# Kernel optimization log

Hardware: AMD Instinct MI355X
Metric: run time of the kernel (lower is better)

## Reference

```python
import jax, jax.numpy as jnp
import numpy as np
from jax import lax

TAU = 2.0
V_TH = 1.0
ALPHA = 4.0   # spikingjelly surrogate.Sigmoid default
BN_EPS = 1e-5
HEADS = 8


def lif(x):
    """Multi-step LIF neuron (tau=2, v_reset=0, hard reset, detach_reset).
    x: [T, ...] -> spikes [T, ...]. Forward is Heaviside; sigmoid surrogate
    is wired in via straight-through for the bwd variant."""
    def step(v, xt):
        v = v + (xt - v) / TAU                      # charge
        sg = jax.nn.sigmoid(ALPHA * (v - V_TH))     # surrogate
        hard = (v >= V_TH).astype(x.dtype)
        spike = sg + lax.stop_gradient(hard - sg)   # fwd: hard, bwd: sigmoid'
        v = v * (1.0 - lax.stop_gradient(spike))    # detached hard reset to 0
        return v, spike
    _, s = lax.scan(step, jnp.zeros_like(x[0]), x)
    return s


def conv1x1_bn(x, w, g, b, m, var, bias=None):
    # x: [N, C, H, W]; 1x1 conv == channel matmul, then eval-mode BN
    y = jnp.einsum('nchw,dc->ndhw', x, w)
    if bias is not None:
        y = y + bias[None, :, None, None]
    scale = g / jnp.sqrt(var + BN_EPS)
    shift = b - m * scale
    return y * scale[None, :, None, None] + shift[None, :, None, None]


def to_heads(x, T, B, C, H, W):
    # [T,B,C,H,W] -> [T,B,heads,N,hd]
    N = H * W
    hd = C // HEADS
    x = x.reshape(T, B, C, N).transpose(0, 1, 3, 2)          # [T,B,N,C]
    return x.reshape(T, B, N, HEADS, hd).transpose(0, 1, 3, 2, 4)


def _forward(x, q_w, q_bn_g, q_bn_b, q_bn_m, q_bn_v,
             k_w, k_bn_g, k_bn_b, k_bn_m, k_bn_v,
             v_w, v_bn_g, v_bn_b, v_bn_m, v_bn_v,
             out_w, out_b, out_bn_g, out_bn_b, out_bn_m, out_bn_v):
    T, B, C, H, W = x.shape
    N = H * W
    identity = x

    xs = lif(x)                                  # shortcut_lif
    x_qkv = xs.reshape(T * B, C, H, W)

    q = lif(conv1x1_bn(x_qkv, q_w, q_bn_g, q_bn_b, q_bn_m, q_bn_v).reshape(T, B, C, H, W))
    k = lif(conv1x1_bn(x_qkv, k_w, k_bn_g, k_bn_b, k_bn_m, k_bn_v).reshape(T, B, C, H, W))
    v = lif(conv1x1_bn(x_qkv, v_w, v_bn_g, v_bn_b, v_bn_m, v_bn_v).reshape(T, B, C, H, W))

    qh = to_heads(q, T, B, C, H, W)              # [T,B,h,N,hd]
    kh = to_heads(k, T, B, C, H, W)
    vh = to_heads(v, T, B, C, H, W)

    kv = jnp.sum(kh * vh, axis=-2, keepdims=True)   # [T,B,h,1,hd]
    kv = lif(kv)                                    # talking_heads_proj_lif
    y = qh * kv                                     # [T,B,h,N,hd]

    # [T,B,h,N,hd] -> transpose(3,4) -> [T,B,h,hd,N] -> [T,B,C,H,W]
    y = y.transpose(0, 1, 2, 4, 3).reshape(T, B, C, H, W)
    y = conv1x1_bn(y.reshape(T * B, C, H, W), out_w, out_bn_g, out_bn_b,
                   out_bn_m, out_bn_v, bias=out_b).reshape(T, B, C, H, W)
    return y + identity, vh


def setup_inputs() -> dict:
    key = jax.random.key(0)
    ks = jax.random.split(key, 6)
    T, B, C, H, W = 4, 32, 512, 14, 14
    inp = {
        'x': jax.random.normal(ks[0], (T, B, C, H, W), dtype=jnp.float32),
        'q_w': jax.random.normal(ks[1], (C, C), dtype=jnp.float32) * 0.05,
        'k_w': jax.random.normal(ks[2], (C, C), dtype=jnp.float32) * 0.05,
        'v_w': jax.random.normal(ks[3], (C, C), dtype=jnp.float32) * 0.05,
        'out_w': jax.random.normal(ks[4], (C, C), dtype=jnp.float32) * 0.05,
        'out_b': jnp.zeros((C,), dtype=jnp.float32),
    }
    for p in ('q', 'k', 'v', 'out'):
        inp[f'{p}_bn_g'] = jnp.ones((C,), dtype=jnp.float32)
        inp[f'{p}_bn_b'] = jnp.zeros((C,), dtype=jnp.float32)
        inp[f'{p}_bn_m'] = jnp.zeros((C,), dtype=jnp.float32)
        inp[f'{p}_bn_v'] = jnp.ones((C,), dtype=jnp.float32)
    return inp


def reference(x, q_w, q_bn_g, q_bn_b, q_bn_m, q_bn_v,
              k_w, k_bn_g, k_bn_b, k_bn_m, k_bn_v,
              v_w, v_bn_g, v_bn_b, v_bn_m, v_bn_v,
              out_w, out_b, out_bn_g, out_bn_b, out_bn_m, out_bn_v):
    return _forward(x, q_w, q_bn_g, q_bn_b, q_bn_m, q_bn_v,
                    k_w, k_bn_g, k_bn_b, k_bn_m, k_bn_v,
                    v_w, v_bn_g, v_bn_b, v_bn_m, v_bn_v,
                    out_w, out_b, out_bn_g, out_bn_b, out_bn_m, out_bn_v)
```

## Files before the change

### kernel.cpp

```cpp
#include <hip/hip_runtime.h>
#include <math.h>

#define T_   4
#define B_   32
#define C_   512
#define N_   196
#define TB_  128
#define M_   25088
#define BNP_ 6272
#define OUT1_ 12845056

typedef unsigned short ushort_t;
typedef __attribute__((ext_vector_type(8)))  __bf16 bf16x8;
typedef __attribute__((ext_vector_type(16))) float  f32x16;

__device__ __forceinline__ ushort_t f2bf(float f) {
    unsigned int u = __float_as_uint(f);
    u = u + 0x7FFFu + ((u >> 16) & 1u);
    return (ushort_t)(u >> 16);
}
__device__ __forceinline__ float bf2f(ushort_t h) {
    return __uint_as_float(((unsigned int)h) << 16);
}

#define GL2LDS(gp, lp) \
    __builtin_amdgcn_global_load_lds((const __attribute__((address_space(1))) void*)(gp), \
                                     (__attribute__((address_space(3))) void*)(lp), 16, 0, 0)

__global__ void prep_kernel(
    const float* __restrict__ qw, const float* __restrict__ kw,
    const float* __restrict__ vw, const float* __restrict__ ow,
    const float* __restrict__ qg, const float* __restrict__ qb, const float* __restrict__ qm, const float* __restrict__ qv,
    const float* __restrict__ kg, const float* __restrict__ kb, const float* __restrict__ km, const float* __restrict__ kvr,
    const float* __restrict__ vg, const float* __restrict__ vb, const float* __restrict__ vm, const float* __restrict__ vv,
    const float* __restrict__ og, const float* __restrict__ ob, const float* __restrict__ om, const float* __restrict__ ov,
    const float* __restrict__ obias,
    ushort_t* __restrict__ wsplit, ushort_t* __restrict__ osplit,
    float* __restrict__ scale_qkv, float* __restrict__ shift_qkv,
    float* __restrict__ scale_o,   float* __restrict__ shift_o,
    float* __restrict__ kvpart)
{
    int i = blockIdx.x * 256 + threadIdx.x;
    int d = i >> 9, c = i & 511;
    const float* src = (d < 512) ? qw : (d < 1024) ? kw : vw;
    float wv = src[(d & 511) * 512 + c];
    ushort_t h = f2bf(wv);
    float r1 = wv - bf2f(h);
    ushort_t mm = f2bf(r1);
    wsplit[((size_t)d * 2 + 0) * 512 + c] = h;
    wsplit[((size_t)d * 2 + 1) * 512 + c] = mm;
    if (d < 512)
        osplit[(size_t)d * 512 + c] = f2bf(ow[d * 512 + c]);

    if (i < 3 * C_) {
        int p = i >> 9, dl = i & 511;
        const float* g = (p == 0) ? qg : (p == 1) ? kg : vg;
        const float* b = (p == 0) ? qb : (p == 1) ? kb : vb;
        const float* m = (p == 0) ? qm : (p == 1) ? km : vm;
        const float* r = (p == 0) ? qv : (p == 1) ? kvr : vv;
        float sc = g[dl] / sqrtf(r[dl] + 1e-5f);
        scale_qkv[i] = sc;
        shift_qkv[i] = b[dl] - m[dl] * sc;
    }
    if (i < C_) {
        float sc = og[i] / sqrtf(ov[i] + 1e-5f);
        scale_o[i] = sc;
        shift_o[i] = ob[i] - om[i] * sc + obias[i] * sc;
    }
    if (i < TB_ * C_) kvpart[i] = 0.f;
}

__global__ __launch_bounds__(256)
void lifx_kernel(const float* __restrict__ x, ushort_t* __restrict__ xs)
{
    __shared__ ushort_t tile[64 * 66];
    const int tid = threadIdx.x;
    const int b = blockIdx.z, c0 = blockIdx.y * 64, n0 = blockIdx.x * 64;
    const int j = tid & 63, w = tid >> 6;
    const bool nok = (n0 + j) < N_;
    float v[16];
#pragma unroll
    for (int r = 0; r < 16; ++r) v[r] = 0.f;
    for (int t = 0; t < T_; ++t) {
        const float* xb = x + ((size_t)((t * B_ + b) * C_ + c0)) * N_ + n0 + j;
#pragma unroll
        for (int r = 0; r < 16; ++r) {
            int i = w * 16 + r;
            float xv = nok ? xb[(size_t)i * N_] : 0.f;
            v[r] = v[r] + (xv - v[r]) * 0.5f;
            bool s = (v[r] >= 1.0f);
            tile[j * 66 + i] = s ? 0x3F80 : 0;
            if (s) v[r] = 0.f;
        }
        __syncthreads();
#pragma unroll
        for (int p = 0; p < 2; ++p) {
            int w2 = tid + p * 256;
            int jj = w2 >> 3, ck = w2 & 7;
            if (n0 + jj < N_) {
                const unsigned int* src = reinterpret_cast<const unsigned int*>(&tile[jj * 66 + ck * 8]);
                uint4 dv; dv.x = src[0]; dv.y = src[1]; dv.z = src[2]; dv.w = src[3];
                size_t mp = (size_t)(b * N_ + n0 + jj) * 4 + t;
                *reinterpret_cast<uint4*>(&xs[mp * 512 + c0 + ck * 8]) = dv;
            }
        }
        __syncthreads();
    }
}

__global__ __launch_bounds__(512, 4)
void qkv_gemm_lif(const ushort_t* __restrict__ W, const ushort_t* __restrict__ X,
                  const float* __restrict__ scale, const float* __restrict__ shift,
                  ushort_t* __restrict__ spk, float* __restrict__ out2)
{
    const int id = blockIdx.x;
    const int xw = id & 7, local = id >> 3;
    const int ml = local / 12, d_t = local - ml * 12;
    const int m_t = ml * 8 + xw;
    if (m_t >= 98) return;
    const int m0 = m_t * 256;
    const int d0 = d_t * 128;

    __shared__ ushort_t Xs[2][16 * 512];
    __shared__ ushort_t Ws[2][16 * 512];
    const int tid = threadIdx.x, wid = tid >> 6, lane = tid & 63;
    const int mw = (wid & 3) * 64, dw = (wid >> 2) * 64;
    const int row32 = lane & 31, khalf = lane >> 5;

    f32x16 acc[2][2] = {};

    auto STAGE = [&](int buf, int k0) {
        {
            int q = wid, mb = q >> 1, ks = q & 1;
            const ushort_t* g = X + (size_t)(m0 + mb * 32 + row32) * 512 + k0 + ks * 16 + khalf * 8;
            GL2LDS(g, &Xs[buf][q * 512]);
        }
        {
            int q = wid + 8, mb = q >> 1, ks = q & 1;
            const ushort_t* g = X + (size_t)(m0 + mb * 32 + row32) * 512 + k0 + ks * 16 + khalf * 8;
            GL2LDS(g, &Xs[buf][q * 512]);
        }
        {
            int q = wid, s = q >> 3, rem = q & 7, db = rem >> 1, ks = rem & 1;
            const ushort_t* g = W + ((size_t)(d0 + db * 32 + row32) * 2 + s) * 512 + k0 + ks * 16 + khalf * 8;
            GL2LDS(g, &Ws[buf][q * 512]);
        }
        {
            int q = wid + 8, s = q >> 3, rem = q & 7, db = rem >> 1, ks = rem & 1;
            const ushort_t* g = W + ((size_t)(d0 + db * 32 + row32) * 2 + s) * 512 + k0 + ks * 16 + khalf * 8;
            GL2LDS(g, &Ws[buf][q * 512]);
        }
    };

    STAGE(0, 0);
    __syncthreads();
    int cur = 0;

    for (int it = 0; it < 16; ++it) {
        if (it < 15) STAGE(cur ^ 1, (it + 1) * 32);

        __builtin_amdgcn_s_setprio(1);
#pragma unroll
        for (int ks = 0; ks < 2; ++ks) {
            bf16x8 xfr[2];
#pragma unroll
            for (int i = 0; i < 2; ++i)
                xfr[i] = *reinterpret_cast<const bf16x8*>(
                    &Xs[cur][(((mw >> 5) + i) * 2 + ks) * 512 + lane * 8]);
#pragma unroll
            for (int s = 0; s < 2; ++s)
#pragma unroll
                for (int j = 0; j < 2; ++j) {
                    bf16x8 wfr = *reinterpret_cast<const bf16x8*>(
                        &Ws[cur][(s * 8 + ((dw >> 5) + j) * 2 + ks) * 512 + lane * 8]);
#pragma unroll
                    for (int i = 0; i < 2; ++i)
                        acc[i][j] = __builtin_amdgcn_mfma_f32_32x32x16_bf16(xfr[i], wfr, acc[i][j], 0, 0, 0);
                }
        }
        __builtin_amdgcn_s_setprio(0);

        __syncthreads();
        cur ^= 1;
    }

    const int p = d0 >> 9;
    const bool isV = (p == 2);
    ushort_t* plane = spk + (size_t)p * ((size_t)M_ * 512);
#pragma unroll
    for (int j = 0; j < 2; ++j) {
        int d = d0 + dw + j * 32 + row32;
        float sc = scale[d], sh = shift[d];
        int dl = d & 511;
        int h = dl >> 6, hd = dl & 63;
#pragma unroll
        for (int i = 0; i < 2; ++i) {
            int bnb = (m0 + mw + i * 32) >> 2;
            f32x16 a = acc[i][j];
#pragma unroll
            for (int g = 0; g < 4; ++g) {
                int bn = bnb + 2 * g + khalf;
                float p0 = fmaf(a[4 * g + 0], sc, sh);
                float p1 = fmaf(a[4 * g + 1], sc, sh);
                float p2 = fmaf(a[4 * g + 2], sc, sh);
                float p3 = fmaf(a[4 * g + 3], sc, sh);
                float v = p0 * 0.5f;
                bool s0 = (v >= 1.f); if (s0) v = 0.f;
                v = v + (p1 - v) * 0.5f;
                bool s1 = (v >= 1.f); if (s1) v = 0.f;
                v = v + (p2 - v) * 0.5f;
                bool s2 = (v >= 1.f); if (s2) v = 0.f;
                v = v + (p3 - v) * 0.5f;
                bool s3 = (v >= 1.f);
                ushort_t* b0 = plane + (size_t)bn * 512 + dl;
                b0[0]                      = s0 ? 0x3F80 : 0;
                b0[(size_t)BNP_ * 512]     = s1 ? 0x3F80 : 0;
                b0[(size_t)2 * BNP_ * 512] = s2 ? 0x3F80 : 0;
                b0[(size_t)3 * BNP_ * 512] = s3 ? 0x3F80 : 0;
                if (isV) {
                    int b = bn / N_, n = bn - b * N_;
                    float* o = out2 + (((size_t)b * 8 + h) * N_ + n) * 64 + hd;
                    o[0]                       = s0 ? 1.f : 0.f;
                    o[(size_t)1 * (OUT1_ / 4)] = s1 ? 1.f : 0.f;
                    o[(size_t)2 * (OUT1_ / 4)] = s2 ? 1.f : 0.f;
                    o[(size_t)3 * (OUT1_ / 4)] = s3 ? 1.f : 0.f;
                }
            }
        }
    }
}

__global__ void kv_part_kernel(const ushort_t* __restrict__ ks, const ushort_t* __restrict__ vs,
                               float* __restrict__ kvpart)
{
    int id = blockIdx.x;
    int tb = id >> 3, r = id & 7;
    int c  = (r & 1) * 256 + threadIdx.x;
    int n0 = (r >> 1) * 49;
    const ushort_t* kb = ks + (size_t)tb * N_ * 512 + c;
    const ushort_t* vb = vs + (size_t)tb * N_ * 512 + c;
    int cnt = 0;
    for (int n = n0; n < n0 + 49; ++n)
        cnt += (kb[(size_t)n * 512] & vb[(size_t)n * 512]) ? 1 : 0;
    atomicAdd(&kvpart[tb * 512 + c], (float)cnt);
}

__global__ void kv_lif_kernel(const float* __restrict__ kvpart, ushort_t* __restrict__ kvs)
{
    int i = blockIdx.x * 256 + threadIdx.x;
    if (i >= B_ * C_) return;
    int b = i >> 9, c = i & 511;
    float v = 0.f;
#pragma unroll
    for (int t = 0; t < T_; ++t) {
        float y = kvpart[((t * B_ + b) << 9) + c];
        v = v + (y - v) * 0.5f;
        bool s = (v >= 1.f);
        kvs[((t * B_ + b) << 9) + c] = s ? 0x3F80 : 0;
        if (s) v = 0.f;
    }
}

__global__ __launch_bounds__(256)
void out_gemm(const ushort_t* __restrict__ A, const ushort_t* __restrict__ qs,
              const ushort_t* __restrict__ kvs,
              const float* __restrict__ scale, const float* __restrict__ shift,
              const float* __restrict__ xid, float* __restrict__ out)
{
    const int id = blockIdx.x;
    const int xw = id & 7, local = id >> 3;
    const int m_t = (local >> 2) * 8 + xw, d_t = local & 3;
    if (m_t >= 196) return;
    const int m0 = m_t * 128, d0 = d_t * 128;

    __shared__ ushort_t As[8 * 512];
    __shared__ ushort_t Bs[8 * 512];
    const int tid = threadIdx.x, wid = tid >> 6, lane = tid & 63;
    const int dw = (wid >> 1) * 64, mw = (wid & 1) * 64;
    const int row32 = lane & 31, khalf = lane >> 5;

    int sm[2], stb[2], sq[2], sL[2];
#pragma unroll
    for (int u = 0; u < 2; ++u) {
        int s = tid + u * 256;
        sq[u] = s >> 6; sL[u] = s & 63;
        sm[u] = m0 + (sq[u] >> 1) * 32 + (sL[u] & 31);
        stb[u] = sm[u] / N_;
    }

    f32x16 acc[2][2] = {};

    for (int k0 = 0; k0 < 512; k0 += 32) {
        __syncthreads();
        for (int q = wid; q < 8; q += 4) {
            int db = q >> 1, ks = q & 1;
            const ushort_t* g = A + (size_t)(d0 + db * 32 + row32) * 512 + k0 + ks * 16 + khalf * 8;
            GL2LDS(g, &As[q * 512]);
        }
#pragma unroll
        for (int u = 0; u < 2; ++u) {
            int kk = k0 + (sq[u] & 1) * 16 + (sL[u] >> 5) * 8;
            uint4 qv = *reinterpret_cast<const uint4*>(&qs[(size_t)sm[u] * 512 + kk]);
            uint4 kv = *reinterpret_cast<const uint4*>(&kvs[(size_t)stb[u] * 512 + kk]);
            uint4 o; o.x = qv.x & kv.x; o.y = qv.y & kv.y; o.z = qv.z & kv.z; o.w = qv.w & kv.w;
            *reinterpret_cast<uint4*>(&Bs[sq[u] * 512 + sL[u] * 8]) = o;
        }
        __syncthreads();

#pragma unroll
        for (int ks = 0; ks < 2; ++ks) {
            bf16x8 afr[2];
#pragma unroll
            for (int i = 0; i < 2; ++i)
                afr[i] = *reinterpret_cast<const bf16x8*>(&As[(((dw >> 5) + i) * 2 + ks) * 512 + lane * 8]);
#pragma unroll
            for (int j = 0; j < 2; ++j) {
                bf16x8 bfr = *reinterpret_cast<const bf16x8*>(&Bs[(((mw >> 5) + j) * 2 + ks) * 512 + lane * 8]);
#pragma unroll
                for (int i = 0; i < 2; ++i)
                    acc[i][j] = __builtin_amdgcn_mfma_f32_32x32x16_bf16(afr[i], bfr, acc[i][j], 0, 0, 0);
            }
        }
    }

#pragma unroll
    for (int j = 0; j < 2; ++j) {
        int m = m0 + mw + j * 32 + row32;
        int tb = m / N_;
        int n  = m - tb * N_;
        size_t mbase = (size_t)tb * (C_ * N_) + n;
#pragma unroll
        for (int i = 0; i < 2; ++i) {
            int dbase = d0 + dw + i * 32 + 4 * khalf;
            f32x16 a = acc[i][j];
#pragma unroll
            for (int g = 0; g < 4; ++g) {
#pragma unroll
                for (int t = 0; t < 4; ++t) {
                    int d = dbase + t + 8 * g;
                    float val = fmaf(a[4 * g + t], scale[d], shift[d]);
                    size_t ad = mbase + (size_t)d * N_;
                    out[ad] = val + xid[ad];
                }
            }
        }
    }
}

extern "C" void kernel_launch(void* const* d_in, const int* in_sizes, int n_in,
                              void* d_out, int out_size, void* d_ws, size_t ws_size,
                              hipStream_t stream)
{
    const float* x    = (const float*)d_in[0];
    const float* q_w  = (const float*)d_in[1];
    const float* k_w  = (const float*)d_in[2];
    const float* v_w  = (const float*)d_in[3];
    const float* o_w  = (const float*)d_in[4];
    const float* o_b  = (const float*)d_in[5];
    const float* qg = (const float*)d_in[6],  *qb = (const float*)d_in[7],
               *qm = (const float*)d_in[8],  *qv = (const float*)d_in[9];
    const float* kg = (const float*)d_in[10], *kb = (const float*)d_in[11],
               *km = (const float*)d_in[12], *kv = (const float*)d_in[13];
    const float* vg = (const float*)d_in[14], *vb = (const float*)d_in[15],
               *vm = (const float*)d_in[16], *vv = (const float*)d_in[17];
    const float* og = (const float*)d_in[18], *ob = (const float*)d_in[19],
               *om = (const float*)d_in[20], *ov = (const float*)d_in[21];

    float* out1  = (float*)d_out;
    float* out2f = out1 + OUT1_;

    ushort_t* spk    = (ushort_t*)d_ws;
    ushort_t* xs     = spk + (size_t)3 * M_ * 512;
    ushort_t* wsplit = xs + (size_t)M_ * 512;
    ushort_t* osplit = wsplit + (size_t)1536 * 2 * 512;
    float*    kvpart = (float*)(osplit + (size_t)512 * 512);
    ushort_t* kvs    = (ushort_t*)(kvpart + TB_ * C_);
    float*    scq    = (float*)(kvs + TB_ * C_);
    float*    shq    = scq + 3 * C_;
    float*    sco    = shq + 3 * C_;
    float*    sho    = sco + C_;

    ushort_t* qsp = spk;
    ushort_t* ksp = spk + (size_t)M_ * 512;
    ushort_t* vsp = spk + (size_t)2 * M_ * 512;

    prep_kernel<<<(1536 * 512) / 256, 256, 0, stream>>>(
        q_w, k_w, v_w, o_w,
        qg, qb, qm, qv, kg, kb, km, kv, vg, vb, vm, vv, og, ob, om, ov, o_b,
        wsplit, osplit, scq, shq, sco, sho, kvpart);

    lifx_kernel<<<dim3(4, 8, 32), 256, 0, stream>>>(x, xs);

    qkv_gemm_lif<<<1200, 512, 0, stream>>>(wsplit, xs, scq, shq, spk, out2f);

    kv_part_kernel<<<1024, 256, 0, stream>>>(ksp, vsp, kvpart);

    kv_lif_kernel<<<64, 256, 0, stream>>>(kvpart, kvs);

    out_gemm<<<800, 256, 0, stream>>>(osplit, qsp, kvs, sco, sho, x, out1);
}
```

Before: 412.0 us.

## Double-buffer out_gemm, relax qkv_gemm barriers, vectorize kv reduction

The out_gemm kernel now double-buffers its A and B tiles in LDS, prefetching the next K slice from global memory while MFMAs run on the current one. qkv_gemm replaces full __syncthreads with explicit vmcnt/lgkmcnt waits and raw barriers, so the prefetch for the next stage can stay in flight. kv_part_kernel is rewritten to read 8 channels per thread with uint4 loads and reduce through LDS atomics, dropping the global float atomics and using fewer blocks. Doubling out_gemm's LDS may lower occupancy, and the hand-written waitcnt values must match the number of outstanding loads for results to stay correct.

```diff
diff --git a/kernel.cpp b/kernel.cpp
--- a/kernel.cpp
+++ b/kernel.cpp
@@ -130,34 +130,36 @@
     f32x16 acc[2][2] = {};
 
     auto STAGE = [&](int buf, int k0) {
-        {
-            int q = wid, mb = q >> 1, ks = q & 1;
+        {   int q = wid, mb = q >> 1, ks = q & 1;
             const ushort_t* g = X + (size_t)(m0 + mb * 32 + row32) * 512 + k0 + ks * 16 + khalf * 8;
             GL2LDS(g, &Xs[buf][q * 512]);
         }
-        {
-            int q = wid + 8, mb = q >> 1, ks = q & 1;
+        {   int q = wid + 8, mb = q >> 1, ks = q & 1;
             const ushort_t* g = X + (size_t)(m0 + mb * 32 + row32) * 512 + k0 + ks * 16 + khalf * 8;
             GL2LDS(g, &Xs[buf][q * 512]);
         }
-        {
-            int q = wid, s = q >> 3, rem = q & 7, db = rem >> 1, ks = rem & 1;
+        {   int q = wid, s = q >> 3, rem = q & 7, db = rem >> 1, ks = rem & 1;
             const ushort_t* g = W + ((size_t)(d0 + db * 32 + row32) * 2 + s) * 512 + k0 + ks * 16 + khalf * 8;
             GL2LDS(g, &Ws[buf][q * 512]);
         }
-        {
-            int q = wid + 8, s = q >> 3, rem = q & 7, db = rem >> 1, ks = rem & 1;
+        {   int q = wid + 8, s = q >> 3, rem = q & 7, db = rem >> 1, ks = rem & 1;
             const ushort_t* g = W + ((size_t)(d0 + db * 32 + row32) * 2 + s) * 512 + k0 + ks * 16 + khalf * 8;
             GL2LDS(g, &Ws[buf][q * 512]);
         }
     };
 
     STAGE(0, 0);
-    __syncthreads();
     int cur = 0;
 
     for (int it = 0; it < 16; ++it) {
-        if (it < 15) STAGE(cur ^ 1, (it + 1) * 32);
+        if (it < 15) {
+            STAGE(cur ^ 1, (it + 1) * 32);
+            asm volatile("s_waitcnt vmcnt(4)" ::: "memory");
+        } else {
+            asm volatile("s_waitcnt vmcnt(0)" ::: "memory");
+        }
+        __builtin_amdgcn_s_barrier();
+        __builtin_amdgcn_sched_barrier(0);
 
         __builtin_amdgcn_s_setprio(1);
 #pragma unroll
@@ -180,7 +182,8 @@
         }
         __builtin_amdgcn_s_setprio(0);
 
-        __syncthreads();
+        asm volatile("s_waitcnt lgkmcnt(0)" ::: "memory");
+        __builtin_amdgcn_s_barrier();
         cur ^= 1;
     }
 
@@ -230,19 +233,34 @@
     }
 }
 
-__global__ void kv_part_kernel(const ushort_t* __restrict__ ks, const ushort_t* __restrict__ vs,
-                               float* __restrict__ kvpart)
-{
-    int id = blockIdx.x;
-    int tb = id >> 3, r = id & 7;
-    int c  = (r & 1) * 256 + threadIdx.x;
-    int n0 = (r >> 1) * 49;
+__global__ __launch_bounds__(256)
+void kv_part_kernel(const ushort_t* __restrict__ ks, const ushort_t* __restrict__ vs,
+                    float* __restrict__ kvpart)
+{
+    __shared__ int cnt[256];
+    const int tid = threadIdx.x;
+    cnt[tid] = 0;
+    __syncthreads();
+    const int tb = blockIdx.x >> 1, ch = blockIdx.x & 1;
+    const int cg = tid & 31, ns = tid >> 5;
+    const int c = ch * 256 + cg * 8;
     const ushort_t* kb = ks + (size_t)tb * N_ * 512 + c;
     const ushort_t* vb = vs + (size_t)tb * N_ * 512 + c;
-    int cnt = 0;
-    for (int n = n0; n < n0 + 49; ++n)
-        cnt += (kb[(size_t)n * 512] & vb[(size_t)n * 512]) ? 1 : 0;
-    atomicAdd(&kvpart[tb * 512 + c], (float)cnt);
+    int loc[8] = {0, 0, 0, 0, 0, 0, 0, 0};
+    int n1 = ns * 25 + 25; if (n1 > N_) n1 = N_;
+    for (int n = ns * 25; n < n1; ++n) {
+        uint4 kq = *reinterpret_cast<const uint4*>(&kb[(size_t)n * 512]);
+        uint4 vq = *reinterpret_cast<const uint4*>(&vb[(size_t)n * 512]);
+        unsigned m;
+        m = kq.x & vq.x; loc[0] += (m & 0xFFFFu) ? 1 : 0; loc[1] += (m >> 16) ? 1 : 0;
+        m = kq.y & vq.y; loc[2] += (m & 0xFFFFu) ? 1 : 0; loc[3] += (m >> 16) ? 1 : 0;
+        m = kq.z & vq.z; loc[4] += (m & 0xFFFFu) ? 1 : 0; loc[5] += (m >> 16) ? 1 : 0;
+        m = kq.w & vq.w; loc[6] += (m & 0xFFFFu) ? 1 : 0; loc[7] += (m >> 16) ? 1 : 0;
+    }
+#pragma unroll
+    for (int e = 0; e < 8; ++e) atomicAdd(&cnt[cg * 8 + e], loc[e]);
+    __syncthreads();
+    kvpart[tb * 512 + ch * 256 + tid] = (float)cnt[tid];
 }
 
 __global__ void kv_lif_kernel(const float* __restrict__ kvpart, ushort_t* __restrict__ kvs)
@@ -273,8 +291,8 @@
     if (m_t >= 196) return;
     const int m0 = m_t * 128, d0 = d_t * 128;
 
-    __shared__ ushort_t As[8 * 512];
-    __shared__ ushort_t Bs[8 * 512];
+    __shared__ ushort_t As[2][8 * 512];
+    __shared__ ushort_t Bs[2][8 * 512];
     const int tid = threadIdx.x, wid = tid >> 6, lane = tid & 63;
     const int dw = (wid >> 1) * 64, mw = (wid & 1) * 64;
     const int row32 = lane & 31, khalf = lane >> 5;
@@ -290,37 +308,75 @@
 
     f32x16 acc[2][2] = {};
 
-    for (int k0 = 0; k0 < 512; k0 += 32) {
-        __syncthreads();
-        for (int q = wid; q < 8; q += 4) {
-            int db = q >> 1, ks = q & 1;
-            const ushort_t* g = A + (size_t)(d0 + db * 32 + row32) * 512 + k0 + ks * 16 + khalf * 8;
-            GL2LDS(g, &As[q * 512]);
-        }
+    {
+        uint4 o[2];
 #pragma unroll
         for (int u = 0; u < 2; ++u) {
-            int kk = k0 + (sq[u] & 1) * 16 + (sL[u] >> 5) * 8;
+            int kk = (sq[u] & 1) * 16 + (sL[u] >> 5) * 8;
             uint4 qv = *reinterpret_cast<const uint4*>(&qs[(size_t)sm[u] * 512 + kk]);
             uint4 kv = *reinterpret_cast<const uint4*>(&kvs[(size_t)stb[u] * 512 + kk]);
-            uint4 o; o.x = qv.x & kv.x; o.y = qv.y & kv.y; o.z = qv.z & kv.z; o.w = qv.w & kv.w;
-            *reinterpret_cast<uint4*>(&Bs[sq[u] * 512 + sL[u] * 8]) = o;
-        }
-        __syncthreads();
-
+            o[u].x = qv.x & kv.x; o[u].y = qv.y & kv.y;
+            o[u].z = qv.z & kv.z; o[u].w = qv.w & kv.w;
+        }
+        for (int q = wid; q < 8; q += 4) {
+            int db = q >> 1, ks2 = q & 1;
+            const ushort_t* g = A + (size_t)(d0 + db * 32 + row32) * 512 + ks2 * 16 + khalf * 8;
+            GL2LDS(g, &As[0][q * 512]);
+        }
+#pragma unroll
+        for (int u = 0; u < 2; ++u)
+            *reinterpret_cast<uint4*>(&Bs[0][sq[u] * 512 + sL[u] * 8]) = o[u];
+    }
+    __syncthreads();
+
+    int buf = 0;
+    for (int it = 0; it < 16; ++it) {
+        uint4 nq[2], nk[2];
+        if (it < 15) {
+            int k0n = (it + 1) * 32;
+#pragma unroll
+            for (int u = 0; u < 2; ++u) {
+                int kk = k0n + (sq[u] & 1) * 16 + (sL[u] >> 5) * 8;
+                nq[u] = *reinterpret_cast<const uint4*>(&qs[(size_t)sm[u] * 512 + kk]);
+                nk[u] = *reinterpret_cast<const uint4*>(&kvs[(size_t)stb[u] * 512 + kk]);
+            }
+            for (int q = wid; q < 8; q += 4) {
+                int db = q >> 1, ks2 = q & 1;
+                const ushort_t* g = A + (size_t)(d0 + db * 32 + row32) * 512 + k0n + ks2 * 16 + khalf * 8;
+                GL2LDS(g, &As[buf ^ 1][q * 512]);
+            }
+        }
+
+        __builtin_amdgcn_s_setprio(1);
 #pragma unroll
         for (int ks = 0; ks < 2; ++ks) {
             bf16x8 afr[2];
 #pragma unroll
             for (int i = 0; i < 2; ++i)
-                afr[i] = *reinterpret_cast<const bf16x8*>(&As[(((dw >> 5) + i) * 2 + ks) * 512 + lane * 8]);
+                afr[i] = *reinterpret_cast<const bf16x8*>(
+                    &As[buf][(((dw >> 5) + i) * 2 + ks) * 512 + lane * 8]);
 #pragma unroll
             for (int j = 0; j < 2; ++j) {
-                bf16x8 bfr = *reinterpret_cast<const bf16x8*>(&Bs[(((mw >> 5) + j) * 2 + ks) * 512 + lane * 8]);
+                bf16x8 bfr = *reinterpret_cast<const bf16x8*>(
+                    &Bs[buf][(((mw >> 5) + j) * 2 + ks) * 512 + lane * 8]);
 #pragma unroll
                 for (int i = 0; i < 2; ++i)
                     acc[i][j] = __builtin_amdgcn_mfma_f32_32x32x16_bf16(afr[i], bfr, acc[i][j], 0, 0, 0);
             }
         }
+        __builtin_amdgcn_s_setprio(0);
+
+        if (it < 15) {
+#pragma unroll
+            for (int u = 0; u < 2; ++u) {
+                uint4 o;
+                o.x = nq[u].x & nk[u].x; o.y = nq[u].y & nk[u].y;
+                o.z = nq[u].z & nk[u].z; o.w = nq[u].w & nk[u].w;
+                *reinterpret_cast<uint4*>(&Bs[buf ^ 1][sq[u] * 512 + sL[u] * 8]) = o;
+            }
+        }
+        __syncthreads();
+        buf ^= 1;
     }
 
 #pragma unroll
@@ -393,7 +449,7 @@
 
     qkv_gemm_lif<<<1200, 512, 0, stream>>>(wsplit, xs, scq, shq, spk, out2f);
 
-    kv_part_kernel<<<1024, 256, 0, stream>>>(ksp, vsp, kvpart);
+    kv_part_kernel<<<256, 256, 0, stream>>>(ksp, vsp, kvpart);
 
     kv_lif_kernel<<<64, 256, 0, stream>>>(kvpart, kvs);
 
```

Result: no change. 407.0 us (-1.2%).
